# Optimization experiments

Measured on AMD Instinct MI355X. Metric: run time of the kernel, lower is better.

The kernel has to match this reference:

```python
import jax, jax.numpy as jnp
import numpy as np

NEG_SLOPE = 0.2


def gatv2(x, src, dst, Wl, Wr, att, b, concat):
    """PyG GATv2Conv (share_weights=False, default negative_slope=0.2).
    x: [N, Fin]; src/dst: [E] (self-loops already included);
    Wl/Wr: [Fin, H*D]; att: [H, D]; b: [H*D] if concat else [D].
    """
    N = x.shape[0]
    H, D = att.shape
    xl = (x @ Wl).reshape(N, H, D)  # source transform (messages)
    xr = (x @ Wr).reshape(N, H, D)  # target transform
    g = xl[src] + xr[dst]                                   # [E, H, D]
    e = jnp.einsum('ehd,hd->eh', jax.nn.leaky_relu(g, NEG_SLOPE), att)  # [E, H]
    # segment softmax over incoming edges of each dst node
    m = jax.ops.segment_max(e, dst, num_segments=N)         # [N, H]
    ex = jnp.exp(e - m[dst])
    s = jax.ops.segment_sum(ex, dst, num_segments=N)
    alpha = ex / (s[dst] + 1e-16)                           # [E, H]
    out = jax.ops.segment_sum(alpha[:, :, None] * xl[src], dst, num_segments=N)  # [N, H, D]
    out = out.reshape(N, H * D) if concat else out.mean(axis=1)
    return out + b


def _glorot(key, fan_in, shape):
    return jax.random.normal(key, shape, dtype=jnp.float32) / np.sqrt(fan_in)


def setup_inputs() -> dict:
    key = jax.random.key(0)
    N, E = 50000, 800000
    dim_in, dim_h, dim_out, heads = 128, 32, 16, 8
    hid = dim_h * heads  # 256
    ks = jax.random.split(key, 16)
    x = jax.random.normal(ks[0], (N, dim_in), dtype=jnp.float32)
    edge_index = jax.random.randint(ks[1], (2, E), 0, N, dtype=jnp.int32)
    p = {
        'Wl1': _glorot(ks[2], dim_in, (dim_in, hid)),
        'Wr1': _glorot(ks[3], dim_in, (dim_in, hid)),
        'att1': _glorot(ks[4], dim_h, (heads, dim_h)),
        'b1': jnp.zeros((hid,), jnp.float32),
        'Wl2': _glorot(ks[5], hid, (hid, hid)),
        'Wr2': _glorot(ks[6], hid, (hid, hid)),
        'att2': _glorot(ks[7], dim_h, (heads, dim_h)),
        'b2': jnp.zeros((hid,), jnp.float32),
        'Wl3': _glorot(ks[8], hid, (hid, hid)),
        'Wr3': _glorot(ks[9], hid, (hid, hid)),
        'att3': _glorot(ks[10], dim_h, (heads, dim_h)),
        'b3': jnp.zeros((hid,), jnp.float32),
        'Wl4': _glorot(ks[11], hid, (hid, dim_out)),
        'Wr4': _glorot(ks[12], hid, (hid, dim_out)),
        'att4': _glorot(ks[13], dim_out, (1, dim_out)),
        'b4': jnp.zeros((dim_out,), jnp.float32),
    }
    return {'x': x, 'edge_index': edge_index, **p}


def reference(x, edge_index,
              Wl1, Wr1, att1, b1,
              Wl2, Wr2, att2, b2,
              Wl3, Wr3, att3, b3,
              Wl4, Wr4, att4, b4):
    N = x.shape[0]
    # PyG GATv2Conv default add_self_loops=True
    loop = jnp.arange(N, dtype=edge_index.dtype)
    src = jnp.concatenate([edge_index[0], loop])
    dst = jnp.concatenate([edge_index[1], loop])
    # eval mode: dropout is identity (note: first dropout output is unused in source)
    h = gatv2(x, src, dst, Wl1, Wr1, att1, b1, concat=True)
    h = jax.nn.elu(h)
    h = gatv2(h, src, dst, Wl2, Wr2, att2, b2, concat=True)
    h = jax.nn.elu(h)
    h = gatv2(h, src, dst, Wl3, Wr3, att3, b3, concat=True)
    h = jax.nn.elu(h)
    h = gatv2(h, src, dst, Wl4, Wr4, att4, b4, concat=True)  # heads=1 -> same as concat
    return jax.nn.log_softmax(h, axis=1)
```

## Files before the change

kernel.cpp:

```cpp
#include <hip/hip_runtime.h>
#include <math.h>

#define NEG_SLOPE 0.2f

typedef _Float16 f16;
typedef _Float16 f16x2 __attribute__((ext_vector_type(2)));
typedef _Float16 f16x4 __attribute__((ext_vector_type(4)));
typedef _Float16 f16x8 __attribute__((ext_vector_type(8)));
typedef float f32x4 __attribute__((ext_vector_type(4)));

static inline int idiv(int a, int b) { return (a + b - 1) / b; }



__global__ __launch_bounds__(256) void conv_x_packed(const float* __restrict__ x,
                                                     f16* __restrict__ pa, int N) {
    int R = blockIdx.x;
    #pragma unroll
    for (int u = 0; u < 8; ++u) {
        int c = threadIdx.x + u * 256;
        int g = c >> 7, r = c & 127;
        int row = R * 128 + r;
        f16x8 v;
        if (row < N) {
            float4 a = *(const float4*)(x + (size_t)row * 128 + g * 8);
            float4 b = *(const float4*)(x + (size_t)row * 128 + g * 8 + 4);
            v = (f16x8){(f16)a.x, (f16)a.y, (f16)a.z, (f16)a.w,
                        (f16)b.x, (f16)b.y, (f16)b.z, (f16)b.w};
        } else {
            v = (f16x8){0, 0, 0, 0, 0, 0, 0, 0};
        }
        *(f16x8*)(pa + ((size_t)(R * 16 + g) * 128 + r) * 8) = v;
    }
}

__global__ __launch_bounds__(256) void convT_all(
    const float* __restrict__ W1l, const float* __restrict__ W1r,
    const float* __restrict__ W2l, const float* __restrict__ W2r,
    const float* __restrict__ W3l, const float* __restrict__ W3r,
    f16* __restrict__ P1l, f16* __restrict__ P1r,
    f16* __restrict__ P2l, f16* __restrict__ P2r,
    f16* __restrict__ P3l, f16* __restrict__ P3r) {
    __shared__ float tbl[32][33];
    const float* W;
    f16* P;
    int K;
    switch (blockIdx.z) {
        case 0: W = W1l; P = P1l; K = 128; break;
        case 1: W = W1r; P = P1r; K = 128; break;
        case 2: W = W2l; P = P2l; K = 256; break;
        case 3: W = W2r; P = P2r; K = 256; break;
        case 4: W = W3l; P = P3l; K = 256; break;
        default: W = W3r; P = P3r; K = 256; break;
    }
    int bk = blockIdx.x * 32, bc = blockIdx.y * 32;
    if (bk >= K) return;
    int tx = threadIdx.x & 31, ty = threadIdx.x >> 5;
    #pragma unroll
    for (int i = 0; i < 32; i += 8)
        tbl[ty + i][tx] = W[(size_t)(bk + ty + i) * 256 + bc + tx];
    __syncthreads();
    if (threadIdx.x < 128) {
        int cl = threadIdx.x & 31;
        int gl = threadIdx.x >> 5;
        int col = bc + cl;
        int g = (bk >> 3) + gl;
        f16x8 v;
        #pragma unroll
        for (int j = 0; j < 8; ++j) v[j] = (f16)tbl[gl * 8 + j][cl];
        *(f16x8*)(P + ((size_t)((col >> 7) * (K >> 3) + g) * 128 + (col & 127)) * 8) = v;
    }
}


__global__ void hist_kernel(const int* __restrict__ dst, int E, int N, int* __restrict__ cnt) {
    int i = blockIdx.x * blockDim.x + threadIdx.x;
    if (i >= E + N) return;
    int d = (i < E) ? dst[i] : (i - E);
    atomicAdd(&cnt[d], 1);
}

__global__ __launch_bounds__(256) void scanA(const int* __restrict__ cnt,
                                             int* __restrict__ bsum, int N) {
    __shared__ int ws[4];
    int tid = threadIdx.x, lane = tid & 63, wid = tid >> 6;
    int i0 = blockIdx.x * 1024 + tid * 4;
    int s = 0;
    if (i0 + 3 < N) {
        int4 v = *(const int4*)(cnt + i0);
        s = v.x + v.y + v.z + v.w;
    } else {
        for (int j = 0; j < 4; ++j)
            if (i0 + j < N) s += cnt[i0 + j];
    }
    #pragma unroll
    for (int o = 1; o < 64; o <<= 1) s += __shfl_xor(s, o);
    if (lane == 0) ws[wid] = s;
    __syncthreads();
    if (tid == 0) bsum[blockIdx.x] = ws[0] + ws[1] + ws[2] + ws[3];
}

__global__ __launch_bounds__(256) void scanB(int* __restrict__ bsum, int nb) {
    __shared__ int ws[4];
    int tid = threadIdx.x, lane = tid & 63, wid = tid >> 6;
    int v = (tid < nb) ? bsum[tid] : 0;
    int incl = v;
    #pragma unroll
    for (int o = 1; o < 64; o <<= 1) {
        int t = __shfl_up(incl, o);
        if (lane >= o) incl += t;
    }
    if (lane == 63) ws[wid] = incl;
    __syncthreads();
    int add = 0;
    for (int w = 0; w < wid; ++w) add += ws[w];
    if (tid < nb) bsum[tid] = add + incl - v;
}

__global__ __launch_bounds__(256) void scanC(const int* __restrict__ cnt,
                                             const int* __restrict__ bsum,
                                             int* __restrict__ rp, int* __restrict__ wofs, int N) {
    __shared__ int ws[4];
    __shared__ int base_s;
    int tid = threadIdx.x, lane = tid & 63, wid = tid >> 6;
    int i0 = blockIdx.x * 1024 + tid * 4;
    int v0 = (i0 + 0 < N) ? cnt[i0 + 0] : 0;
    int v1 = (i0 + 1 < N) ? cnt[i0 + 1] : 0;
    int v2 = (i0 + 2 < N) ? cnt[i0 + 2] : 0;
    int v3 = (i0 + 3 < N) ? cnt[i0 + 3] : 0;
    int t4 = v0 + v1 + v2 + v3;
    int incl = t4;
    #pragma unroll
    for (int o = 1; o < 64; o <<= 1) {
        int t = __shfl_up(incl, o);
        if (lane >= o) incl += t;
    }
    if (lane == 63) ws[wid] = incl;
    if (tid == 0) base_s = bsum[blockIdx.x];
    __syncthreads();
    int wadd = 0;
    for (int w = 0; w < wid; ++w) wadd += ws[w];
    int pre = base_s + wadd + incl - t4;
    int p1 = pre + v0, p2 = p1 + v1, p3 = p2 + v2, p4 = p3 + v3;
    if (i0 + 0 < N) { wofs[i0 + 0] = pre; rp[i0 + 1] = p1; }
    if (i0 + 1 < N) { wofs[i0 + 1] = p1;  rp[i0 + 2] = p2; }
    if (i0 + 2 < N) { wofs[i0 + 2] = p2;  rp[i0 + 3] = p3; }
    if (i0 + 3 < N) { wofs[i0 + 3] = p3;  rp[i0 + 4] = p4; }
    if (blockIdx.x == 0 && tid == 0) rp[0] = 0;
}

__global__ void scatter_kernel(const int* __restrict__ src, const int* __restrict__ dst,
                               int E, int N, int* __restrict__ wofs, int* __restrict__ sorted_src) {
    int i = blockIdx.x * blockDim.x + threadIdx.x;
    if (i >= E + N) return;
    int d, s;
    if (i < E) { d = dst[i]; s = src[i]; } else { d = i - E; s = d; }
    int pos = atomicAdd(&wofs[d], 1);
    sorted_src[pos] = s;
}


__device__ __forceinline__ void gll16(const f16* g, f16* l) {
#if __has_builtin(__builtin_amdgcn_global_load_lds)
    __builtin_amdgcn_global_load_lds((const __attribute__((address_space(1))) void*)g,
                                     (__attribute__((address_space(3))) void*)l, 16, 0, 0);
#else
    *(f16x8*)l = *(const f16x8*)g;
#endif
}

__global__ __launch_bounds__(256) void gemm16_packed(
    const f16* __restrict__ PA, int N, int K,
    const f16* __restrict__ PBl, const f16* __restrict__ PBr,
    f16* __restrict__ Cl, f16* __restrict__ Cr) {
    __shared__ f16 lds[2][2][8192];
    const int nblk = gridDim.x;
    int bid = blockIdx.x;
    int xcd = bid & 7, jj = bid >> 3;
    int nper = nblk >> 3, rem = nblk & 7;
    int slot = (xcd < rem) ? xcd * (nper + 1) + jj
                           : rem * (nper + 1) + (xcd - rem) * nper + jj;
    int R = slot >> 2, by = slot & 3;
    const f16* __restrict__ PB = (by >> 1) ? PBr : PBl;
    f16* __restrict__ C = (by >> 1) ? Cr : Cl;
    const int cb = by & 1;
    const int row0 = R * 128;
    const f16* Abase = PA + (size_t)R * 128 * K;
    const f16* Bbase = PB + (size_t)cb * 128 * K;
    const int t = threadIdx.x;
    const int lane = t & 63, wid = t >> 6;
    const int wr = (wid >> 1) * 64, wc = (wid & 1) * 64;
    const int lg = lane >> 4, lr = lane & 15;

    f32x4 acc[4][4];
    #pragma unroll
    for (int m = 0; m < 4; ++m)
        #pragma unroll
        for (int n = 0; n < 4; ++n) acc[m][n] = (f32x4){0.f, 0.f, 0.f, 0.f};

    auto stage = [&](int buf, int k0) {
        const f16* As = Abase + (size_t)k0 * 128 + t * 8;
        const f16* Bs = Bbase + (size_t)k0 * 128 + t * 8;
        f16* Al = &lds[buf][0][t * 8];
        f16* Bl = &lds[buf][1][t * 8];
        #pragma unroll
        for (int u = 0; u < 4; ++u) gll16(As + u * 2048, Al + u * 2048);
        #pragma unroll
        for (int u = 0; u < 4; ++u) gll16(Bs + u * 2048, Bl + u * 2048);
    };

    const int nk = K >> 6;
    stage(0, 0);
    asm volatile("s_waitcnt vmcnt(0)" ::: "memory");
    __syncthreads();
    for (int c = 0; c < nk; ++c) {
        if (c + 1 < nk) stage((c + 1) & 1, (c + 1) * 64);
        f16x8* Asp = (f16x8*)lds[c & 1][0];
        f16x8* Bsp = (f16x8*)lds[c & 1][1];
        #pragma unroll
        for (int s = 0; s < 2; ++s) {
            f16x8 af[4], bf[4];
            #pragma unroll
            for (int m = 0; m < 4; ++m) af[m] = Asp[(s * 4 + lg) * 128 + wr + m * 16 + lr];
            #pragma unroll
            for (int n = 0; n < 4; ++n) bf[n] = Bsp[(s * 4 + lg) * 128 + wc + n * 16 + lr];
            #pragma unroll
            for (int m = 0; m < 4; ++m)
                #pragma unroll
                for (int n = 0; n < 4; ++n)
                    acc[m][n] = __builtin_amdgcn_mfma_f32_16x16x32_f16(af[m], bf[n], acc[m][n], 0, 0, 0);
        }
        asm volatile("s_waitcnt vmcnt(0)" ::: "memory");
        __syncthreads();
    }
    f16* ldsc = &lds[0][0][0];
    #pragma unroll
    for (int m = 0; m < 4; ++m) {
        #pragma unroll
        for (int reg = 0; reg < 4; ++reg) {
            int row = wr + m * 16 + lg * 4 + reg;
            int sw = (row & 7) << 3;
            #pragma unroll
            for (int n = 0; n < 4; ++n) {
                int col = wc + n * 16 + lr;
                ldsc[row * 128 + (col ^ sw)] = (f16)acc[m][n][reg];
            }
        }
    }
    __syncthreads();
    const size_t hs = (size_t)N * 32;
    #pragma unroll
    for (int u = 0; u < 8; ++u) {
        int idx = u * 256 + t;
        int hh = idx >> 9;
        int rem = idx & 511;
        int r = rem >> 2;
        int cc = (rem & 3) << 3;
        int col = hh * 32 + cc;
        f16x8 v = *(const f16x8*)&ldsc[r * 128 + (col ^ ((r & 7) << 3))];
        int grow = row0 + r;
        if (grow < N)
            *(f16x8*)(C + hs * (cb * 4 + hh) + (size_t)grow * 32 + cc) = v;
    }
}


__global__ __launch_bounds__(256) void gemm_small16(
    const f16* __restrict__ A, int N,
    const float* __restrict__ Wl, const float* __restrict__ Wr,
    float* __restrict__ Cl, float* __restrict__ Cr) {
    const int K = 256, M = 16;
    __shared__ float As[16][260];
    __shared__ float Ws[256 * 16];
    const float* __restrict__ W = (blockIdx.y == 0) ? Wl : Wr;
    float* __restrict__ C = (blockIdx.y == 0) ? Cl : Cr;
    int row0 = blockIdx.x * 16;
    int tid = threadIdx.x;
    {
        #pragma unroll
        for (int u = 0; u < 4; ++u)
            *(float4*)&Ws[tid * 16 + u * 4] = *(const float4*)(W + tid * 16 + u * 4);
        int r = tid >> 4;
        int c = (tid & 15) * 16;
        int row = row0 + r;
        if (row < N) {
            int R = row >> 7, rr = row & 127;
            const f16* base = A + ((size_t)(R * 32 + (c >> 3)) * 128 + rr) * 8;
            f16x8 v0 = *(const f16x8*)base;
            f16x8 v1 = *(const f16x8*)(base + 1024);
            #pragma unroll
            for (int j = 0; j < 8; ++j) {
                As[r][c + j] = (float)v0[j];
                As[r][c + 8 + j] = (float)v1[j];
            }
        } else {
            #pragma unroll
            for (int j = 0; j < 16; ++j) As[r][c + j] = 0.f;
        }
    }
    __syncthreads();
    int r = tid >> 4;
    int col = tid & 15;
    float acc = 0.f;
    #pragma unroll 8
    for (int k = 0; k < K; ++k) acc = fmaf(As[r][k], Ws[k * M + col], acc);
    int row = row0 + r;
    if (row < N) C[(size_t)row * M + col] = acc;
}


__global__ __launch_bounds__(256) void edge_h8_ns(
    const f16* __restrict__ xl, const f16* __restrict__ xr,
    const int* __restrict__ rp, const int* __restrict__ ss,
    const float* __restrict__ att, const float* __restrict__ bias,
    f16* __restrict__ hout, int N) {
    int bid = blockIdx.x;
    int h = bid & 7;
    int tile = bid >> 3;
    int tid = threadIdx.x;
    int n = tile * 64 + (tid >> 2);
    if (n >= N) return;
    int ll = tid & 3;
    const size_t hs = (size_t)N * 32;
    const f16* xlh = xl + hs * h;
    const int doff = h * 32 + ll * 8;
    f16x8 xrr = *(const f16x8*)(xr + hs * h + (size_t)n * 32 + ll * 8);
    float4 atlo = *(const float4*)(att + doff);
    float4 athi = *(const float4*)(att + doff + 4);
    f16x2 at01 = {(f16)atlo.x, (f16)atlo.y};
    f16x2 at23 = {(f16)atlo.z, (f16)atlo.w};
    f16x2 at45 = {(f16)athi.x, (f16)athi.y};
    f16x2 at67 = {(f16)athi.z, (f16)athi.w};
    const f16 ns = (f16)NEG_SLOPE;
    float m = -INFINITY, s = 0.f;
    f16x8 a = {0, 0, 0, 0, 0, 0, 0, 0};
    int beg = rp[n], end = rp[n + 1];
    int last = end - 1;
    const f16* xb = xlh + ll * 8;
    f16x8 r0 = *(const f16x8*)(xb + (size_t)ss[beg] * 32);
    f16x8 r1 = *(const f16x8*)(xb + (size_t)ss[min(beg + 1, last)] * 32);
    f16x8 r2 = *(const f16x8*)(xb + (size_t)ss[min(beg + 2, last)] * 32);
    f16x8 r3 = *(const f16x8*)(xb + (size_t)ss[min(beg + 3, last)] * 32);
    int j4 = ss[min(beg + 4, last)];
    int j5 = ss[min(beg + 5, last)];

    auto score = [&](const f16x8& cur) -> float {
        f16x8 g = cur + xrr;
        f16x8 gs = g * ns;
        f16x8 lk = __builtin_elementwise_max(g, gs);
#if __has_builtin(__builtin_amdgcn_fdot2)
        f16x2 l01 = __builtin_shufflevector(lk, lk, 0, 1);
        f16x2 l23 = __builtin_shufflevector(lk, lk, 2, 3);
        f16x2 l45 = __builtin_shufflevector(lk, lk, 4, 5);
        f16x2 l67 = __builtin_shufflevector(lk, lk, 6, 7);
        float p = __builtin_amdgcn_fdot2(l01, at01, 0.f, false);
        p = __builtin_amdgcn_fdot2(l23, at23, p, false);
        p = __builtin_amdgcn_fdot2(l45, at45, p, false);
        p = __builtin_amdgcn_fdot2(l67, at67, p, false);
#else
        float p = (float)lk[0] * atlo.x + (float)lk[1] * atlo.y +
                  (float)lk[2] * atlo.z + (float)lk[3] * atlo.w +
                  (float)lk[4] * athi.x + (float)lk[5] * athi.y +
                  (float)lk[6] * athi.z + (float)lk[7] * athi.w;
#endif
        return p;
    };

    int i = beg;
    for (; i + 1 < end; i += 2) {
        f16x8 c0 = r0, c1 = r1;
        r0 = r2; r1 = r3;
        r2 = *(const f16x8*)(xb + (size_t)j4 * 32);
        r3 = *(const f16x8*)(xb + (size_t)j5 * 32);
        j4 = ss[min(i + 6, last)];
        j5 = ss[min(i + 7, last)];
        float p0 = score(c0);
        float p1 = score(c1);
        p0 += __shfl_xor(p0, 1);
        p1 += __shfl_xor(p1, 1);
        p0 += __shfl_xor(p0, 2);
        p1 += __shfl_xor(p1, 2);
        float d0 = p0 - m, d1 = p1 - m;
        if (__any(fmaxf(d0, d1) > 4.f)) {
            float mn = fmaxf(m, fmaxf(p0, p1));
            float cf = __expf(m - mn);
            s *= cf;
            f16 cfh = (f16)cf;
            a = a * (f16x8){cfh, cfh, cfh, cfh, cfh, cfh, cfh, cfh};
            m = mn;
            d0 = p0 - m; d1 = p1 - m;
        }
        float e0 = __expf(d0);
        float e1 = __expf(d1);
        s += e0 + e1;
        f16 e0h = (f16)e0, e1h = (f16)e1;
        f16x8 e0v = {e0h, e0h, e0h, e0h, e0h, e0h, e0h, e0h};
        f16x8 e1v = {e1h, e1h, e1h, e1h, e1h, e1h, e1h, e1h};
#if __has_builtin(__builtin_elementwise_fma)
        a = __builtin_elementwise_fma(c0, e0v, a);
        a = __builtin_elementwise_fma(c1, e1v, a);
#else
        a = a + c0 * e0v + c1 * e1v;
#endif
    }
    if (i < end) {
        f16x8 c0 = r0;
        float p0 = score(c0);
        p0 += __shfl_xor(p0, 1);
        p0 += __shfl_xor(p0, 2);
        float d0 = p0 - m;
        if (__any(d0 > 4.f)) {
            float mn = fmaxf(m, p0);
            float cf = __expf(m - mn);
            s *= cf;
            f16 cfh = (f16)cf;
            a = a * (f16x8){cfh, cfh, cfh, cfh, cfh, cfh, cfh, cfh};
            m = mn;
            d0 = p0 - m;
        }
        float e0 = __expf(d0);
        s += e0;
        f16 e0h = (f16)e0;
        f16x8 e0v = {e0h, e0h, e0h, e0h, e0h, e0h, e0h, e0h};
#if __has_builtin(__builtin_elementwise_fma)
        a = __builtin_elementwise_fma(c0, e0v, a);
#else
        a = a + c0 * e0v;
#endif
    }
    float inv = 1.f / (s + 1e-16f);
    float4 blo = *(const float4*)(bias + doff);
    float4 bhi = *(const float4*)(bias + doff + 4);
    float o[8];
    o[0] = (float)a[0] * inv + blo.x; o[1] = (float)a[1] * inv + blo.y;
    o[2] = (float)a[2] * inv + blo.z; o[3] = (float)a[3] * inv + blo.w;
    o[4] = (float)a[4] * inv + bhi.x; o[5] = (float)a[5] * inv + bhi.y;
    o[6] = (float)a[6] * inv + bhi.z; o[7] = (float)a[7] * inv + bhi.w;
    f16x8 ov;
    #pragma unroll
    for (int j = 0; j < 8; ++j) {
        float e = o[j] > 0.f ? o[j] : __expf(o[j]) - 1.f;
        ov[j] = (f16)e;
    }
    *(f16x8*)(hout + ((size_t)((n >> 7) * 32 + 4 * h + ll) * 128 + (n & 127)) * 8) = ov;
}


__global__ __launch_bounds__(256) void edge_h1_kernel(
    const float* __restrict__ xl, const float* __restrict__ xr,
    const int* __restrict__ rp, const int* __restrict__ ss,
    const float* __restrict__ att, const float* __restrict__ bias,
    float* __restrict__ out, int N) {
    int tid = threadIdx.x;
    int grp = tid >> 4;
    int gl = tid & 15;
    int n = blockIdx.x * 16 + grp;
    if (n >= N) return;
    float xrv = xr[(size_t)n * 16 + gl];
    float attv = att[gl];
    float bv = bias[gl];
    float m = -INFINITY, s = 0.f, acc = 0.f;
    int beg = rp[n], end = rp[n + 1], last = end - 1;
    const float* xb = xl + gl;
    float x0 = xb[(size_t)ss[beg] * 16];
    float x1 = xb[(size_t)ss[min(beg + 1, last)] * 16];
    float x2 = xb[(size_t)ss[min(beg + 2, last)] * 16];
    float x3 = xb[(size_t)ss[min(beg + 3, last)] * 16];
    int j4 = ss[min(beg + 4, last)];
    int j5 = ss[min(beg + 5, last)];
    int i = beg;
    for (; i + 1 < end; i += 2) {
        float c0 = x0, c1 = x1;
        x0 = x2; x1 = x3;
        x2 = xb[(size_t)j4 * 16];
        x3 = xb[(size_t)j5 * 16];
        j4 = ss[min(i + 6, last)];
        j5 = ss[min(i + 7, last)];
        float g0 = c0 + xrv, g1 = c1 + xrv;
        float p0 = attv * fmaxf(g0, NEG_SLOPE * g0);
        float p1 = attv * fmaxf(g1, NEG_SLOPE * g1);
        p0 += __shfl_xor(p0, 1); p1 += __shfl_xor(p1, 1);
        p0 += __shfl_xor(p0, 2); p1 += __shfl_xor(p1, 2);
        p0 += __shfl_xor(p0, 4); p1 += __shfl_xor(p1, 4);
        p0 += __shfl_xor(p0, 8); p1 += __shfl_xor(p1, 8);
        float d0 = p0 - m, d1 = p1 - m;
        if (__any(fmaxf(d0, d1) > 8.f)) {
            float mn = fmaxf(m, fmaxf(p0, p1));
            float cf = __expf(m - mn);
            s *= cf; acc *= cf;
            m = mn;
            d0 = p0 - m; d1 = p1 - m;
        }
        float e0 = __expf(d0), e1 = __expf(d1);
        s += e0 + e1;
        acc = fmaf(e1, c1, fmaf(e0, c0, acc));
    }
    if (i < end) {
        float c0 = x0;
        float g0 = c0 + xrv;
        float p0 = attv * fmaxf(g0, NEG_SLOPE * g0);
        p0 += __shfl_xor(p0, 1);
        p0 += __shfl_xor(p0, 2);
        p0 += __shfl_xor(p0, 4);
        p0 += __shfl_xor(p0, 8);
        float d0 = p0 - m;
        if (__any(d0 > 8.f)) {
            float mn = fmaxf(m, p0);
            float cf = __expf(m - mn);
            s *= cf; acc *= cf;
            m = mn;
            d0 = p0 - m;
        }
        float e0 = __expf(d0);
        s += e0;
        acc = fmaf(e0, c0, acc);
    }
    float v = acc / (s + 1e-16f) + bv;
    float mx = v;
    mx = fmaxf(mx, __shfl_xor(mx, 1));
    mx = fmaxf(mx, __shfl_xor(mx, 2));
    mx = fmaxf(mx, __shfl_xor(mx, 4));
    mx = fmaxf(mx, __shfl_xor(mx, 8));
    float ex = __expf(v - mx);
    float se = ex;
    se += __shfl_xor(se, 1);
    se += __shfl_xor(se, 2);
    se += __shfl_xor(se, 4);
    se += __shfl_xor(se, 8);
    out[(size_t)n * 16 + gl] = v - mx - __logf(se);
}


extern "C" void kernel_launch(void* const* d_in, const int* in_sizes, int n_in,
                              void* d_out, int out_size, void* d_ws, size_t ws_size,
                              hipStream_t stream) {
    const float* x    = (const float*)d_in[0];
    const int*   ei   = (const int*)d_in[1];
    const float* Wl1  = (const float*)d_in[2];
    const float* Wr1  = (const float*)d_in[3];
    const float* att1 = (const float*)d_in[4];
    const float* b1   = (const float*)d_in[5];
    const float* Wl2  = (const float*)d_in[6];
    const float* Wr2  = (const float*)d_in[7];
    const float* att2 = (const float*)d_in[8];
    const float* b2   = (const float*)d_in[9];
    const float* Wl3  = (const float*)d_in[10];
    const float* Wr3  = (const float*)d_in[11];
    const float* att3 = (const float*)d_in[12];
    const float* b3   = (const float*)d_in[13];
    const float* Wl4  = (const float*)d_in[14];
    const float* Wr4  = (const float*)d_in[15];
    const float* att4 = (const float*)d_in[16];
    const float* b4   = (const float*)d_in[17];

    const int N = in_sizes[0] / 128;
    const int E = in_sizes[1] / 2;
    const int* src = ei;
    const int* dst = ei + E;
    const int Etot = E + N;
    const int ntile = idiv(N, 128);

    char* wsb = (char*)d_ws;
    size_t off = 0;
    auto alloc = [&](size_t bytes) -> void* {
        void* p = wsb + off;
        off += (bytes + 255) & ~(size_t)255;
        return p;
    };
    f16*   PX   = (f16*)alloc((size_t)ntile * 128 * 128 * 2);
    f16*   PH   = (f16*)alloc((size_t)ntile * 128 * 256 * 2);
    f16*   xl16 = (f16*)alloc((size_t)N * 256 * 2);
    f16*   xr16 = (f16*)alloc((size_t)N * 256 * 2);
    float* xl4  = (float*)alloc((size_t)N * 16 * 4);
    float* xr4  = (float*)alloc((size_t)N * 16 * 4);
    f16*   PB1l = (f16*)alloc((size_t)256 * 128 * 2);
    f16*   PB1r = (f16*)alloc((size_t)256 * 128 * 2);
    f16*   PB2l = (f16*)alloc((size_t)256 * 256 * 2);
    f16*   PB2r = (f16*)alloc((size_t)256 * 256 * 2);
    f16*   PB3l = (f16*)alloc((size_t)256 * 256 * 2);
    f16*   PB3r = (f16*)alloc((size_t)256 * 256 * 2);
    int*   cnt  = (int*)alloc((size_t)N * 4);
    int*   wof  = (int*)alloc((size_t)N * 4);
    int*   rp   = (int*)alloc((size_t)(N + 1) * 4);
    int*   ss   = (int*)alloc((size_t)Etot * 4);
    int*   bsum = (int*)alloc((size_t)idiv(N, 1024) * 4);

    conv_x_packed<<<ntile, 256, 0, stream>>>(x, PX, N);
    convT_all<<<dim3(8, 8, 6), 256, 0, stream>>>(Wl1, Wr1, Wl2, Wr2, Wl3, Wr3,
                                                 PB1l, PB1r, PB2l, PB2r, PB3l, PB3r);

    hipMemsetAsync(cnt, 0, (size_t)N * 4, stream);
    hist_kernel<<<idiv(Etot, 256), 256, 0, stream>>>(dst, E, N, cnt);
    const int nb = idiv(N, 1024);
    scanA<<<nb, 256, 0, stream>>>(cnt, bsum, N);
    scanB<<<1, 256, 0, stream>>>(bsum, nb);
    scanC<<<nb, 256, 0, stream>>>(cnt, bsum, rp, wof, N);
    scatter_kernel<<<idiv(Etot, 256), 256, 0, stream>>>(src, dst, E, N, wof, ss);

    const int nblk = ntile * 4;
    const int egrid = idiv(N, 64) * 8;
    gemm16_packed<<<nblk, 256, 0, stream>>>(PX, N, 128, PB1l, PB1r, xl16, xr16);
    edge_h8_ns<<<egrid, 256, 0, stream>>>(xl16, xr16, rp, ss, att1, b1, PH, N);
    gemm16_packed<<<nblk, 256, 0, stream>>>(PH, N, 256, PB2l, PB2r, xl16, xr16);
    edge_h8_ns<<<egrid, 256, 0, stream>>>(xl16, xr16, rp, ss, att2, b2, PH, N);
    gemm16_packed<<<nblk, 256, 0, stream>>>(PH, N, 256, PB3l, PB3r, xl16, xr16);
    edge_h8_ns<<<egrid, 256, 0, stream>>>(xl16, xr16, rp, ss, att3, b3, PH, N);
    gemm_small16<<<dim3(idiv(N, 16), 2), 256, 0, stream>>>(PH, N, Wl4, Wr4, xl4, xr4);
    edge_h1_kernel<<<idiv(N, 16), 256, 0, stream>>>(xl4, xr4, rp, ss, att4, b4,
                                                    (float*)d_out, N);
}
```

Measured before the change: 440.2 us.

## Split fused edge softmax into separate score and aggregation kernels

```diff
diff --git a/kernel.cpp b/kernel.cpp
--- a/kernel.cpp
+++ b/kernel.cpp
@@ -150,13 +150,15 @@
 }
 
 __global__ void scatter_kernel(const int* __restrict__ src, const int* __restrict__ dst,
-                               int E, int N, int* __restrict__ wofs, int* __restrict__ sorted_src) {
+                               int E, int N, int* __restrict__ wofs,
+                               int* __restrict__ sorted_src, int* __restrict__ sorted_dst) {
     int i = blockIdx.x * blockDim.x + threadIdx.x;
     if (i >= E + N) return;
     int d, s;
     if (i < E) { d = dst[i]; s = src[i]; } else { d = i - E; s = d; }
     int pos = atomicAdd(&wofs[d], 1);
     sorted_src[pos] = s;
+    sorted_dst[pos] = d;
 }
 
 
@@ -253,9 +255,9 @@
     for (int u = 0; u < 8; ++u) {
         int idx = u * 256 + t;
         int hh = idx >> 9;
-        int rem = idx & 511;
-        int r = rem >> 2;
-        int cc = (rem & 3) << 3;
+        int rem2 = idx & 511;
+        int r = rem2 >> 2;
+        int cc = (rem2 & 3) << 3;
         int col = hh * 32 + cc;
         f16x8 v = *(const f16x8*)&ldsc[r * 128 + (col ^ ((r & 7) << 3))];
         int grow = row0 + r;
@@ -309,11 +311,62 @@
 }
 
 
-__global__ __launch_bounds__(256) void edge_h8_ns(
+__global__ __launch_bounds__(256) void edge_score(
     const f16* __restrict__ xl, const f16* __restrict__ xr,
-    const int* __restrict__ rp, const int* __restrict__ ss,
-    const float* __restrict__ att, const float* __restrict__ bias,
-    f16* __restrict__ hout, int N) {
+    const int* __restrict__ ss, const int* __restrict__ sd,
+    const float* __restrict__ att, f16* __restrict__ esc, int Ep, int N) {
+    int bid = blockIdx.x;
+    int h = bid & 7;
+    int chunk = bid >> 3;
+    const size_t hs = (size_t)N * 32;
+    const f16* xlh = xl + hs * h;
+    const f16* xrh = xr + hs * h;
+    f16* eh = esc + (size_t)h * Ep;
+    f16x2 at[16];
+    #pragma unroll
+    for (int j = 0; j < 16; ++j) {
+        float2 av = *(const float2*)(att + h * 32 + j * 2);
+        at[j] = (f16x2){(f16)av.x, (f16)av.y};
+    }
+    const f16 ns = (f16)NEG_SLOPE;
+    int base = chunk * 1024 + threadIdx.x;
+    #pragma unroll 1
+    for (int u = 0; u < 4; ++u) {
+        int i = base + u * 256;
+        if (i >= Ep) break;
+        int sidx = ss[i], didx = sd[i];
+        const f16* pl = xlh + (size_t)sidx * 32;
+        const f16* pr = xrh + (size_t)didx * 32;
+        float p = 0.f;
+        #pragma unroll
+        for (int q = 0; q < 4; ++q) {
+            f16x8 cl = *(const f16x8*)(pl + q * 8);
+            f16x8 cr = *(const f16x8*)(pr + q * 8);
+            f16x8 g = cl + cr;
+            f16x8 gs = g * ns;
+            f16x8 lk = __builtin_elementwise_max(g, gs);
+#if __has_builtin(__builtin_amdgcn_fdot2)
+            #pragma unroll
+            for (int w = 0; w < 4; ++w) {
+                f16x2 l2 = {lk[w * 2], lk[w * 2 + 1]};
+                p = __builtin_amdgcn_fdot2(l2, at[q * 4 + w], p, false);
+            }
+#else
+            #pragma unroll
+            for (int w = 0; w < 8; ++w)
+                p += (float)lk[w] * (float)(w & 1 ? at[q * 4 + (w >> 1)][1]
+                                                  : at[q * 4 + (w >> 1)][0]);
+#endif
+        }
+        eh[i] = (f16)p;
+    }
+}
+
+
+__global__ __launch_bounds__(256) void edge_agg(
+    const f16* __restrict__ xl, const int* __restrict__ rp,
+    const int* __restrict__ ss, const f16* __restrict__ esc,
+    const float* __restrict__ bias, f16* __restrict__ hout, int Ep, int N) {
     int bid = blockIdx.x;
     int h = bid & 7;
     int tile = bid >> 3;
@@ -322,50 +375,23 @@
     if (n >= N) return;
     int ll = tid & 3;
     const size_t hs = (size_t)N * 32;
-    const f16* xlh = xl + hs * h;
+    const f16* xb = xl + hs * h + ll * 8;
+    const f16* eh = esc + (size_t)h * Ep;
     const int doff = h * 32 + ll * 8;
-    f16x8 xrr = *(const f16x8*)(xr + hs * h + (size_t)n * 32 + ll * 8);
-    float4 atlo = *(const float4*)(att + doff);
-    float4 athi = *(const float4*)(att + doff + 4);
-    f16x2 at01 = {(f16)atlo.x, (f16)atlo.y};
-    f16x2 at23 = {(f16)atlo.z, (f16)atlo.w};
-    f16x2 at45 = {(f16)athi.x, (f16)athi.y};
-    f16x2 at67 = {(f16)athi.z, (f16)athi.w};
-    const f16 ns = (f16)NEG_SLOPE;
-    float m = -INFINITY, s = 0.f;
-    f16x8 a = {0, 0, 0, 0, 0, 0, 0, 0};
     int beg = rp[n], end = rp[n + 1];
+    float mv = -INFINITY;
+    for (int j = beg + ll; j < end; j += 4) mv = fmaxf(mv, (float)eh[j]);
+    mv = fmaxf(mv, __shfl_xor(mv, 1));
+    mv = fmaxf(mv, __shfl_xor(mv, 2));
     int last = end - 1;
-    const f16* xb = xlh + ll * 8;
     f16x8 r0 = *(const f16x8*)(xb + (size_t)ss[beg] * 32);
     f16x8 r1 = *(const f16x8*)(xb + (size_t)ss[min(beg + 1, last)] * 32);
     f16x8 r2 = *(const f16x8*)(xb + (size_t)ss[min(beg + 2, last)] * 32);
     f16x8 r3 = *(const f16x8*)(xb + (size_t)ss[min(beg + 3, last)] * 32);
     int j4 = ss[min(beg + 4, last)];
     int j5 = ss[min(beg + 5, last)];
-
-    auto score = [&](const f16x8& cur) -> float {
-        f16x8 g = cur + xrr;
-        f16x8 gs = g * ns;
-        f16x8 lk = __builtin_elementwise_max(g, gs);
-#if __has_builtin(__builtin_amdgcn_fdot2)
-        f16x2 l01 = __builtin_shufflevector(lk, lk, 0, 1);
-        f16x2 l23 = __builtin_shufflevector(lk, lk, 2, 3);
-        f16x2 l45 = __builtin_shufflevector(lk, lk, 4, 5);
-        f16x2 l67 = __builtin_shufflevector(lk, lk, 6, 7);
-        float p = __builtin_amdgcn_fdot2(l01, at01, 0.f, false);
-        p = __builtin_amdgcn_fdot2(l23, at23, p, false);
-        p = __builtin_amdgcn_fdot2(l45, at45, p, false);
-        p = __builtin_amdgcn_fdot2(l67, at67, p, false);
-#else
-        float p = (float)lk[0] * atlo.x + (float)lk[1] * atlo.y +
-                  (float)lk[2] * atlo.z + (float)lk[3] * atlo.w +
-                  (float)lk[4] * athi.x + (float)lk[5] * athi.y +
-                  (float)lk[6] * athi.z + (float)lk[7] * athi.w;
-#endif
-        return p;
-    };
-
+    float s = 0.f;
+    f16x8 a = {0, 0, 0, 0, 0, 0, 0, 0};
     int i = beg;
     for (; i + 1 < end; i += 2) {
         f16x8 c0 = r0, c1 = r1;
@@ -374,24 +400,8 @@
         r3 = *(const f16x8*)(xb + (size_t)j5 * 32);
         j4 = ss[min(i + 6, last)];
         j5 = ss[min(i + 7, last)];
-        float p0 = score(c0);
-        float p1 = score(c1);
-        p0 += __shfl_xor(p0, 1);
-        p1 += __shfl_xor(p1, 1);
-        p0 += __shfl_xor(p0, 2);
-        p1 += __shfl_xor(p1, 2);
-        float d0 = p0 - m, d1 = p1 - m;
-        if (__any(fmaxf(d0, d1) > 4.f)) {
-            float mn = fmaxf(m, fmaxf(p0, p1));
-            float cf = __expf(m - mn);
-            s *= cf;
-            f16 cfh = (f16)cf;
-            a = a * (f16x8){cfh, cfh, cfh, cfh, cfh, cfh, cfh, cfh};
-            m = mn;
-            d0 = p0 - m; d1 = p1 - m;
-        }
-        float e0 = __expf(d0);
-        float e1 = __expf(d1);
+        float e0 = __expf((float)eh[i] - mv);
+        float e1 = __expf((float)eh[i + 1] - mv);
         s += e0 + e1;
         f16 e0h = (f16)e0, e1h = (f16)e1;
         f16x8 e0v = {e0h, e0h, e0h, e0h, e0h, e0h, e0h, e0h};
@@ -405,20 +415,7 @@
     }
     if (i < end) {
         f16x8 c0 = r0;
-        float p0 = score(c0);
-        p0 += __shfl_xor(p0, 1);
-        p0 += __shfl_xor(p0, 2);
-        float d0 = p0 - m;
-        if (__any(d0 > 4.f)) {
-            float mn = fmaxf(m, p0);
-            float cf = __expf(m - mn);
-            s *= cf;
-            f16 cfh = (f16)cf;
-            a = a * (f16x8){cfh, cfh, cfh, cfh, cfh, cfh, cfh, cfh};
-            m = mn;
-            d0 = p0 - m;
-        }
-        float e0 = __expf(d0);
+        float e0 = __expf((float)eh[i] - mv);
         s += e0;
         f16 e0h = (f16)e0;
         f16x8 e0v = {e0h, e0h, e0h, e0h, e0h, e0h, e0h, e0h};
@@ -583,6 +580,8 @@
     int*   wof  = (int*)alloc((size_t)N * 4);
     int*   rp   = (int*)alloc((size_t)(N + 1) * 4);
     int*   ss   = (int*)alloc((size_t)Etot * 4);
+    int*   sd   = (int*)alloc((size_t)Etot * 4);
+    f16*   esc  = (f16*)alloc((size_t)8 * Etot * 2);
     int*   bsum = (int*)alloc((size_t)idiv(N, 1024) * 4);
 
     conv_x_packed<<<ntile, 256, 0, stream>>>(x, PX, N);
@@ -595,16 +594,20 @@
     scanA<<<nb, 256, 0, stream>>>(cnt, bsum, N);
     scanB<<<1, 256, 0, stream>>>(bsum, nb);
     scanC<<<nb, 256, 0, stream>>>(cnt, bsum, rp, wof, N);
-    scatter_kernel<<<idiv(Etot, 256), 256, 0, stream>>>(src, dst, E, N, wof, ss);
+    scatter_kernel<<<idiv(Etot, 256), 256, 0, stream>>>(src, dst, E, N, wof, ss, sd);
 
     const int nblk = ntile * 4;
-    const int egrid = idiv(N, 64) * 8;
+    const int sgrid = idiv(Etot, 1024) * 8;
+    const int agrid = idiv(N, 64) * 8;
     gemm16_packed<<<nblk, 256, 0, stream>>>(PX, N, 128, PB1l, PB1r, xl16, xr16);
-    edge_h8_ns<<<egrid, 256, 0, stream>>>(xl16, xr16, rp, ss, att1, b1, PH, N);
+    edge_score<<<sgrid, 256, 0, stream>>>(xl16, xr16, ss, sd, att1, esc, Etot, N);
+    edge_agg<<<agrid, 256, 0, stream>>>(xl16, rp, ss, esc, b1, PH, Etot, N);
     gemm16_packed<<<nblk, 256, 0, stream>>>(PH, N, 256, PB2l, PB2r, xl16, xr16);
-    edge_h8_ns<<<egrid, 256, 0, stream>>>(xl16, xr16, rp, ss, att2, b2, PH, N);
+    edge_score<<<sgrid, 256, 0, stream>>>(xl16, xr16, ss, sd, att2, esc, Etot, N);
+    edge_agg<<<agrid, 256, 0, stream>>>(xl16, rp, ss, esc, b2, PH, Etot, N);
     gemm16_packed<<<nblk, 256, 0, stream>>>(PH, N, 256, PB3l, PB3r, xl16, xr16);
-    edge_h8_ns<<<egrid, 256, 0, stream>>>(xl16, xr16, rp, ss, att3, b3, PH, N);
+    edge_score<<<sgrid, 256, 0, stream>>>(xl16, xr16, ss, sd, att3, esc, Etot, N);
+    edge_agg<<<agrid, 256, 0, stream>>>(xl16, rp, ss, esc, b3, PH, Etot, N);
     gemm_small16<<<dim3(idiv(N, 16), 2), 256, 0, stream>>>(PH, N, Wl4, Wr4, xl4, xr4);
     edge_h1_kernel<<<idiv(N, 16), 256, 0, stream>>>(xl4, xr4, rp, ss, att4, b4,
                                                     (float*)d_out, N);
```

New measurement: 627.5 us. +42.5%, slower.
